# Optimization experiments

Measured on AMD Instinct MI355X. Metric: run time of the kernel, lower is better.

The kernel has to match this reference:

```python
import jax, jax.numpy as jnp
import numpy as np

DIM = 256
N_EMBED = 8192
DECAY = 0.99
EPS = 1e-05


def setup_inputs() -> dict:
    key = jax.random.key(0)
    k1, k2, k3, k4 = jax.random.split(key, 4)
    z = jax.random.normal(k1, (16, 32, 32, DIM), dtype=jnp.float32)
    embedding = jax.random.normal(k2, (DIM, N_EMBED), dtype=jnp.float32)
    cluster_size = jax.random.uniform(k3, (N_EMBED,), dtype=jnp.float32)
    embedding_avg = jax.random.normal(k4, (DIM, N_EMBED), dtype=jnp.float32)
    return {"z": z, "embedding": embedding, "cluster_size": cluster_size,
            "embedding_avg": embedding_avg}


def reference(z, embedding, cluster_size, embedding_avg):
    flatten = z.reshape(-1, DIM)  # [N, dim]
    dist = ((flatten ** 2).sum(1, keepdims=True)
            - 2.0 * flatten @ embedding
            + (embedding ** 2).sum(0, keepdims=True))
    embed_ind_flat = jnp.argmin(dist, axis=1)  # [N] int
    embed_ind = embed_ind_flat.reshape(z.shape[:-1])
    # Gather codes: embedding is [dim, n_embed]; quantize [..., dim]
    quantize = jnp.take(embedding.T, embed_ind_flat, axis=0).reshape(z.shape)

    # EMA codebook update (training path), via segment sums (no dense one-hot)
    onehot_sum = jax.ops.segment_sum(
        jnp.ones_like(embed_ind_flat, dtype=flatten.dtype),
        embed_ind_flat, num_segments=N_EMBED)  # [n_embed]
    embed_sum = jax.ops.segment_sum(flatten, embed_ind_flat,
                                    num_segments=N_EMBED).T  # [dim, n_embed]
    new_cluster_size = cluster_size * DECAY + (1.0 - DECAY) * onehot_sum
    new_embedding_avg = embedding_avg * DECAY + (1.0 - DECAY) * embed_sum
    n = new_cluster_size.sum()
    smoothed = (new_cluster_size + EPS) / (n + N_EMBED * EPS) * n
    new_embedding = new_embedding_avg / smoothed[None, :]

    diff = jnp.mean((jax.lax.stop_gradient(quantize) - z) ** 2)
    quantize_st = z + jax.lax.stop_gradient(quantize - z)
    return (quantize_st, diff, embed_ind, new_embedding,
            new_cluster_size, new_embedding_avg)
```

## Files before the change

kernel.cpp:

```cpp
#include <hip/hip_runtime.h>


#define DIMC  256
#define NEMB  8192
#define NROWS 16384

#define OUT_Q      0u
#define OUT_DIFF   4194304u
#define OUT_IDX    4194305u
#define OUT_NEWEMB 4210689u
#define OUT_NEWCS  6307841u
#define OUT_NEWAVG 6316033u

#define WS_EHI    0u
#define WS_ELO    1048576u
#define WS_COUNT  2097152u
#define WS_DIFF   2105344u
#define WS_N      2105345u
#define WS_ENORM  2105346u
#define WS_PACK   2113540u

typedef __attribute__((ext_vector_type(8))) short short8;
typedef __attribute__((ext_vector_type(4))) float f32x4;

__device__ inline void split_bf16(float x, unsigned short& h, unsigned short& l) {
  unsigned u = __float_as_uint(x);
  unsigned r = u + 0x7FFFu + ((u >> 16) & 1u);
  h = (unsigned short)(r >> 16);
  float hf = __uint_as_float((unsigned)h << 16);
  float lo = x - hf;
  unsigned u2 = __float_as_uint(lo);
  unsigned r2 = u2 + 0x7FFFu + ((u2 >> 16) & 1u);
  l = (unsigned short)(r2 >> 16);
}

__device__ inline float bf16_f(unsigned short u) {
  return __uint_as_float((unsigned)u << 16);
}

__global__ __launch_bounds__(256) void prep_kernel(
    const float* __restrict__ z, const float* __restrict__ emb,
    const float* __restrict__ cs, unsigned short* __restrict__ z_hi,
    unsigned short* __restrict__ z_lo, unsigned short* __restrict__ e_hi,
    unsigned short* __restrict__ e_lo, float* __restrict__ enorm,
    float* __restrict__ embsum, unsigned long long* __restrict__ pack,
    float* __restrict__ count_diff, float* __restrict__ n_out) {
  const int b = blockIdx.x;
  const int t = threadIdx.x;
  __shared__ float tile[64][68];
  __shared__ float red[4][64];

  if (b < 1024) {
#pragma unroll
    for (int it = 0; it < 4; ++it) {
      const int idx = (b * 256 + t) + it * 262144;
      const float4 v = reinterpret_cast<const float4*>(z)[idx];
      ushort4 h, l;
      split_bf16(v.x, h.x, l.x);
      split_bf16(v.y, h.y, l.y);
      split_bf16(v.z, h.z, l.z);
      split_bf16(v.w, h.w, l.w);
      reinterpret_cast<ushort4*>(z_hi)[idx] = h;
      reinterpret_cast<ushort4*>(z_lo)[idx] = l;
    }
  } else if (b < 1536) {
    const int bb = b - 1024;
    const int n0 = (bb & 127) * 64;
    const int k0 = (bb >> 7) * 64;
    const int c4 = (t & 15) * 4;
    const int rr = t >> 4;
#pragma unroll
    for (int i = 0; i < 4; ++i) {
      const int kl = rr + i * 16;
      const float4 v = *reinterpret_cast<const float4*>(
          &emb[(size_t)(k0 + kl) * NEMB + n0 + c4]);
      *reinterpret_cast<float4*>(&tile[kl][c4]) = v;
    }
    __syncthreads();
#pragma unroll
    for (int i = 0; i < 4; ++i) {
      const int nr = rr + i * 16;
      float4 v;
      v.x = tile[c4 + 0][nr];
      v.y = tile[c4 + 1][nr];
      v.z = tile[c4 + 2][nr];
      v.w = tile[c4 + 3][nr];
      const size_t off = (size_t)(n0 + nr) * DIMC + k0 + c4;
      ushort4 h, l;
      split_bf16(v.x, h.x, l.x);
      split_bf16(v.y, h.y, l.y);
      split_bf16(v.z, h.z, l.z);
      split_bf16(v.w, h.w, l.w);
      *reinterpret_cast<ushort4*>(&e_hi[off]) = h;
      *reinterpret_cast<ushort4*>(&e_lo[off]) = l;
    }
  } else if (b < 2048) {
    const int bb = b - 1536;
    const float4 zero = {0.f, 0.f, 0.f, 0.f};
#pragma unroll
    for (int it = 0; it < 4; ++it)
      reinterpret_cast<float4*>(embsum)[bb * 1024 + t + it * 256] = zero;
  } else if (b < 2176) {
    const int l = t & 63;
    const int dg = t >> 6;
    const int e = (b - 2048) * 64 + l;
    float s = 0.f;
#pragma unroll 8
    for (int d = dg * 64; d < dg * 64 + 64; ++d) {
      const float v = emb[(size_t)d * NEMB + e];
      s = fmaf(v, v, s);
    }
    red[dg][l] = s;
    __syncthreads();
    if (dg == 0) enorm[e] = red[0][l] + red[1][l] + red[2][l] + red[3][l];
  } else if (b < 2184) {
    const int bb = b - 2176;
    const uint4 ff = {~0u, ~0u, ~0u, ~0u};
#pragma unroll
    for (int it = 0; it < 4; ++it)
      reinterpret_cast<uint4*>(pack)[bb * 1024 + t + it * 256] = ff;
  } else if (b == 2184) {
    for (int i = t; i < 8193; i += 256) count_diff[i] = 0.f;
  } else {
    float s = 0.f;
#pragma unroll
    for (int i = 0; i < 32; ++i) s += cs[t + i * 256];
#pragma unroll
    for (int off = 32; off > 0; off >>= 1) s += __shfl_down(s, off, 64);
    if ((t & 63) == 0) red[0][t >> 6] = s;
    __syncthreads();
    if (t == 0)
      n_out[0] = 0.99f * (red[0][0] + red[0][1] + red[0][2] + red[0][3]) +
                 163.84f;
  }
}

__global__ __launch_bounds__(256, 2) void argmin_mfma_kernel(
    const unsigned short* __restrict__ z_hi, const unsigned short* __restrict__ z_lo,
    const unsigned short* __restrict__ e_hi, const unsigned short* __restrict__ e_lo,
    const float* __restrict__ enorm, unsigned long long* __restrict__ pack) {
  __shared__ short za[16384];
  __shared__ short eb[16384];
  __shared__ float elds[2048];
  const int tid = threadIdx.x;
  const int bid = blockIdx.x;
  const int xcd = bid & 7;
  const int w = bid >> 3;
  const int r0 = (xcd * 16 + (w & 15)) * 128;
  const int ebase = (w >> 4) * 2048;
  const int tx = tid & 15;
  const int q = (tid >> 4) & 3;
  const int wave = tid >> 6;
  const int wm = wave & 1;
  const int wn = wave >> 1;

  const unsigned zdel = (unsigned)(z_lo - z_hi);
  const unsigned edel = (unsigned)(e_lo - e_hi);

  const int lp = (tid & 7) ^ ((tid >> 3) & 7);
  const unsigned sz = (lp & 4) ? zdel : 0u;
  const unsigned se = (lp & 4) ? edel : 0u;
  const unsigned dch8 = (unsigned)(lp & 3) * 8u;
  unsigned zo[4], eo[4];
#pragma unroll
  for (int it = 0; it < 4; ++it) {
    const int row_it = (tid >> 3) + it * 32;
    zo[it] = sz + (unsigned)(r0 + row_it) * 256u + dch8;
    eo[it] = se + (unsigned)(ebase + row_it) * 256u + dch8;
  }

  auto STAGE = [&](int sidx) {
    const unsigned k0s = (unsigned)(sidx & 7) * 32u;
    const unsigned eas = (unsigned)(sidx >> 3) * 32768u + k0s;
    const unsigned lb = (unsigned)(sidx & 1) * 8192u + (unsigned)tid * 8u;
#pragma unroll
    for (int it = 0; it < 4; ++it) {
      __builtin_amdgcn_global_load_lds(
          (const __attribute__((address_space(1))) unsigned int*)(z_hi + zo[it] + k0s),
          (__attribute__((address_space(3))) unsigned int*)&za[lb + it * 2048],
          16, 0, 0);
      __builtin_amdgcn_global_load_lds(
          (const __attribute__((address_space(1))) unsigned int*)(e_hi + eo[it] + eas),
          (__attribute__((address_space(3))) unsigned int*)&eb[lb + it * 2048],
          16, 0, 0);
    }
  };

  float rmin[4][4];
  int ridx[4][4];
#pragma unroll
  for (int i = 0; i < 4; ++i)
#pragma unroll
    for (int r = 0; r < 4; ++r) { rmin[i][r] = 3.4028235e38f; ridx[i][r] = 0; }

  STAGE(0);
  {
    const float4 v0 = *reinterpret_cast<const float4*>(&enorm[ebase + tid * 8]);
    const float4 v1 =
        *reinterpret_cast<const float4*>(&enorm[ebase + tid * 8 + 4]);
    *reinterpret_cast<float4*>(&elds[tid * 8]) = v0;
    *reinterpret_cast<float4*>(&elds[tid * 8 + 4]) = v1;
  }
  __syncthreads();

  for (int nt = 0; nt < 16; ++nt) {
    f32x4 acc[4][4];
#pragma unroll
    for (int i = 0; i < 4; ++i)
#pragma unroll
      for (int j = 0; j < 4; ++j) acc[i][j] = (f32x4)0.0f;

    for (int k2 = 0; k2 < 8; ++k2) {
      const int s = nt * 8 + k2;
      if (s < 127) STAGE(s + 1);

      const short* zb = &za[(unsigned)(s & 1) * 8192u];
      const short* ebf = &eb[(unsigned)(s & 1) * 8192u];
      short8 ah[4], al[4], bh[4], bl[4];
#pragma unroll
      for (int i = 0; i < 4; ++i) {
        const int va = q ^ (tx & 7);
        const int rl = wm * 64 + i * 16 + tx;
        ah[i] = *reinterpret_cast<const short8*>(&zb[rl * 64 + va * 8]);
        al[i] = *reinterpret_cast<const short8*>(&zb[rl * 64 + (va ^ 4) * 8]);
        const int cl = wn * 64 + i * 16 + tx;
        bh[i] = *reinterpret_cast<const short8*>(&ebf[cl * 64 + va * 8]);
        bl[i] = *reinterpret_cast<const short8*>(&ebf[cl * 64 + (va ^ 4) * 8]);
      }
#pragma unroll
      for (int i = 0; i < 4; ++i)
#pragma unroll
        for (int j = 0; j < 4; ++j) {
          acc[i][j] = __builtin_amdgcn_mfma_f32_16x16x32_bf16(ah[i], bh[j],
                                                             acc[i][j], 0, 0, 0);
          acc[i][j] = __builtin_amdgcn_mfma_f32_16x16x32_bf16(ah[i], bl[j],
                                                             acc[i][j], 0, 0, 0);
          acc[i][j] = __builtin_amdgcn_mfma_f32_16x16x32_bf16(al[i], bh[j],
                                                             acc[i][j], 0, 0, 0);
        }

      asm volatile("s_waitcnt vmcnt(0) lgkmcnt(0)" ::: "memory");
      __builtin_amdgcn_sched_barrier(0);
      __builtin_amdgcn_s_barrier();
      asm volatile("" ::: "memory");
    }

#pragma unroll
    for (int j = 0; j < 4; ++j) {
      const int cidx = nt * 128 + wn * 64 + j * 16 + tx;
      const float en = elds[cidx];
      const int col = ebase + cidx;
#pragma unroll
      for (int i = 0; i < 4; ++i)
#pragma unroll
        for (int r = 0; r < 4; ++r) {
          const float sc = en - 2.0f * acc[i][j][r];
          if (sc < rmin[i][r]) { rmin[i][r] = sc; ridx[i][r] = col; }
        }
    }
  }

#pragma unroll
  for (int i = 0; i < 4; ++i)
#pragma unroll
    for (int r = 0; r < 4; ++r) {
      float v = rmin[i][r];
      int ix = ridx[i][r];
#pragma unroll
      for (int off = 1; off < 16; off <<= 1) {
        const float ov = __shfl_xor(v, off, 16);
        const int oi = __shfl_xor(ix, off, 16);
        if (ov < v || (ov == v && oi < ix)) { v = ov; ix = oi; }
      }
      if (tx == 0) {
        const unsigned int fb = __float_as_uint(v);
        const unsigned int sb = (fb & 0x80000000u) ? ~fb : (fb | 0x80000000u);
        const unsigned long long key =
            ((unsigned long long)sb << 13) | (unsigned long long)(unsigned)ix;
        atomicMin(&pack[r0 + wm * 64 + i * 16 + q * 4 + r], key);
      }
    }
}

__global__ __launch_bounds__(256) void gather_update_kernel(
    const float* __restrict__ z, const unsigned short* __restrict__ e_hi,
    const unsigned short* __restrict__ e_lo,
    const unsigned long long* __restrict__ pack, float* __restrict__ out_q,
    float* __restrict__ out_idx, float* __restrict__ embsum,
    float* __restrict__ count, float* __restrict__ diff_acc) {
  const int row = blockIdx.x * 4 + (threadIdx.x >> 6);
  const int lane = threadIdx.x & 63;
  const int e = (int)(pack[row] & 8191ULL);
  if (lane == 0) out_idx[row] = (float)e;
  const float4 zv =
      *reinterpret_cast<const float4*>(&z[(size_t)row * DIMC + lane * 4]);
  const ushort4 h =
      *reinterpret_cast<const ushort4*>(&e_hi[(size_t)e * DIMC + lane * 4]);
  const ushort4 l =
      *reinterpret_cast<const ushort4*>(&e_lo[(size_t)e * DIMC + lane * 4]);
  const float q0 = bf16_f(h.x) + bf16_f(l.x);
  const float q1 = bf16_f(h.y) + bf16_f(l.y);
  const float q2 = bf16_f(h.z) + bf16_f(l.z);
  const float q3 = bf16_f(h.w) + bf16_f(l.w);
  const float d0 = q0 - zv.x, d1 = q1 - zv.y, d2 = q2 - zv.z, d3 = q3 - zv.w;
  float4 st;
  st.x = zv.x + d0; st.y = zv.y + d1; st.z = zv.z + d2; st.w = zv.w + d3;
  *reinterpret_cast<float4*>(&out_q[(size_t)row * DIMC + lane * 4]) = st;

  atomicAdd(&embsum[(size_t)e * DIMC + lane * 4 + 0], zv.x);
  atomicAdd(&embsum[(size_t)e * DIMC + lane * 4 + 1], zv.y);
  atomicAdd(&embsum[(size_t)e * DIMC + lane * 4 + 2], zv.z);
  atomicAdd(&embsum[(size_t)e * DIMC + lane * 4 + 3], zv.w);

  float local = d0 * d0 + d1 * d1 + d2 * d2 + d3 * d3;
#pragma unroll
  for (int off = 32; off > 0; off >>= 1) local += __shfl_down(local, off, 64);

  __shared__ float dred[4];
  if (lane == 0) {
    dred[threadIdx.x >> 6] = local;
    atomicAdd(&count[e], 1.0f);
  }
  __syncthreads();
  if (threadIdx.x == 0)
    atomicAdd(diff_acc, dred[0] + dred[1] + dred[2] + dred[3]);
}

__global__ __launch_bounds__(256) void fin1_kernel(
    const float* __restrict__ eavg, const float* __restrict__ embsum,
    const float* __restrict__ cs, const float* __restrict__ count,
    const float* __restrict__ n_ptr, const float* __restrict__ diff_acc,
    float* __restrict__ out_emb, float* __restrict__ out_ncs,
    float* __restrict__ out_diff) {
  const int b = blockIdx.x;
  const int t = threadIdx.x;
  __shared__ float tile[64][68];
  __shared__ float rs[64];
  if (b < 512) {
    const int e0 = (b & 127) * 64;
    const int d0 = (b >> 7) * 64;
    const int c4 = (t & 15) * 4;
    const int rr = t >> 4;
    if (t < 64) {
      const float n = n_ptr[0];
      const float ncs = cs[e0 + t] * 0.99f + 0.01f * count[e0 + t];
      const float sm = (ncs + 1e-5f) / (n + 0.08192f) * n;
      rs[t] = 1.0f / sm;
    }
#pragma unroll
    for (int i = 0; i < 4; ++i) {
      const int er = rr + i * 16;
      const float4 v = *reinterpret_cast<const float4*>(
          &embsum[(size_t)(e0 + er) * DIMC + d0 + c4]);
      *reinterpret_cast<float4*>(&tile[er][c4]) = v;
    }
    __syncthreads();
#pragma unroll
    for (int i = 0; i < 4; ++i) {
      const int dr = rr + i * 16;
      const size_t g = (size_t)(d0 + dr) * NEMB + e0 + c4;
      const float4 av = *reinterpret_cast<const float4*>(&eavg[g]);
      float4 o;
      o.x = (av.x * 0.99f + 0.01f * tile[c4 + 0][dr]) * rs[c4 + 0];
      o.y = (av.y * 0.99f + 0.01f * tile[c4 + 1][dr]) * rs[c4 + 1];
      o.z = (av.z * 0.99f + 0.01f * tile[c4 + 2][dr]) * rs[c4 + 2];
      o.w = (av.w * 0.99f + 0.01f * tile[c4 + 3][dr]) * rs[c4 + 3];
      *reinterpret_cast<float4*>(&out_emb[g]) = o;
    }
  } else {
    const int g = (b - 512) * 256 + t;
    out_ncs[g] = cs[g] * 0.99f + 0.01f * count[g];
    if (g == 0) out_diff[0] = diff_acc[0] * (1.0f / 4194304.0f);
  }
}

__global__ __launch_bounds__(256) void fin2b_kernel(
    const float* __restrict__ cs, const float* __restrict__ count,
    const float* __restrict__ n_ptr, const float* __restrict__ out_emb,
    float* __restrict__ out_avg) {
  const int g = blockIdx.x * 256 + threadIdx.x;
  const int e = g & 8191;
  const float n = n_ptr[0];
  const float ncs = cs[e] * 0.99f + 0.01f * count[e];
  const float sm = (ncs + 1e-5f) / (n + 0.08192f) * n;
  out_avg[g] = out_emb[g] * sm;
}

extern "C" void kernel_launch(void* const* d_in, const int* in_sizes, int n_in,
                              void* d_out, int out_size, void* d_ws,
                              size_t ws_size, hipStream_t stream) {
  const float* z = (const float*)d_in[0];
  const float* emb = (const float*)d_in[1];
  const float* cs = (const float*)d_in[2];
  const float* eavg = (const float*)d_in[3];
  float* out = (float*)d_out;
  float* ws = (float*)d_ws;

  unsigned short* e_hi = (unsigned short*)(ws + WS_EHI);
  unsigned short* e_lo = (unsigned short*)(ws + WS_ELO);
  float* ws_count = ws + WS_COUNT;
  float* ws_diff = ws + WS_DIFF;
  float* ws_n = ws + WS_N;
  float* ws_enorm = ws + WS_ENORM;
  unsigned long long* ws_pack = (unsigned long long*)(ws + WS_PACK);

  unsigned short* z_hi = (unsigned short*)(out + OUT_Q);
  unsigned short* z_lo = (unsigned short*)(out + OUT_Q + 2097152);
  float* embsum = out + OUT_NEWAVG;

  prep_kernel<<<2186, 256, 0, stream>>>(z, emb, cs, z_hi, z_lo, e_hi, e_lo,
                                        ws_enorm, embsum, ws_pack, ws_count,
                                        ws_n);
  argmin_mfma_kernel<<<512, 256, 0, stream>>>(z_hi, z_lo, e_hi, e_lo, ws_enorm,
                                              ws_pack);
  gather_update_kernel<<<NROWS / 4, 256, 0, stream>>>(
      z, e_hi, e_lo, ws_pack, out + OUT_Q, out + OUT_IDX, embsum, ws_count,
      ws_diff);
  fin1_kernel<<<544, 256, 0, stream>>>(eavg, embsum, cs, ws_count, ws_n,
                                       ws_diff, out + OUT_NEWEMB,
                                       out + OUT_NEWCS, out + OUT_DIFF);
  fin2b_kernel<<<(DIMC * NEMB) / 256, 256, 0, stream>>>(
      cs, ws_count, ws_n, out + OUT_NEWEMB, out + OUT_NEWAVG);
}
```

Before: 384.9 us.

## Load codebook operands directly from global into registers, dropping LDS staging

The codebook (B) tiles are no longer staged through LDS. Each wave loads its bf16 hi/lo fragments directly from global memory into double-buffered registers one step ahead, while z still goes through LDS. The k2 loop is fully unrolled and the per-step wait drops the lgkmcnt and sched_barrier. This halves LDS footprint and traffic, which may allow more occupancy, but it duplicates global/L2 reads of the codebook across waves. Uncoalesced per-lane 16-byte loads and extra register pressure may also hurt. The final stage wraps around to prefetch redundant data instead of skipping.

Result: slower. 535.3 us (+39.1%).

```diff
diff --git a/kernel.cpp b/kernel.cpp
--- a/kernel.cpp
+++ b/kernel.cpp
@@ -140,7 +140,6 @@
     const unsigned short* __restrict__ e_hi, const unsigned short* __restrict__ e_lo,
     const float* __restrict__ enorm, unsigned long long* __restrict__ pack) {
   __shared__ short za[16384];
-  __shared__ short eb[16384];
   __shared__ float elds[2048];
   const int tid = threadIdx.x;
   const int bid = blockIdx.x;
@@ -153,25 +152,23 @@
   const int wave = tid >> 6;
   const int wm = wave & 1;
   const int wn = wave >> 1;
+  const int va = q ^ (tx & 7);
+  const unsigned qa8 = (unsigned)q * 8u;
 
   const unsigned zdel = (unsigned)(z_lo - z_hi);
-  const unsigned edel = (unsigned)(e_lo - e_hi);
 
   const int lp = (tid & 7) ^ ((tid >> 3) & 7);
   const unsigned sz = (lp & 4) ? zdel : 0u;
-  const unsigned se = (lp & 4) ? edel : 0u;
   const unsigned dch8 = (unsigned)(lp & 3) * 8u;
-  unsigned zo[4], eo[4];
+  unsigned zo[4];
 #pragma unroll
   for (int it = 0; it < 4; ++it) {
     const int row_it = (tid >> 3) + it * 32;
     zo[it] = sz + (unsigned)(r0 + row_it) * 256u + dch8;
-    eo[it] = se + (unsigned)(ebase + row_it) * 256u + dch8;
-  }
-
-  auto STAGE = [&](int sidx) {
+  }
+
+  auto STAGE_Z = [&](int sidx) {
     const unsigned k0s = (unsigned)(sidx & 7) * 32u;
-    const unsigned eas = (unsigned)(sidx >> 3) * 32768u + k0s;
     const unsigned lb = (unsigned)(sidx & 1) * 8192u + (unsigned)tid * 8u;
 #pragma unroll
     for (int it = 0; it < 4; ++it) {
@@ -179,10 +176,6 @@
           (const __attribute__((address_space(1))) unsigned int*)(z_hi + zo[it] + k0s),
           (__attribute__((address_space(3))) unsigned int*)&za[lb + it * 2048],
           16, 0, 0);
-      __builtin_amdgcn_global_load_lds(
-          (const __attribute__((address_space(1))) unsigned int*)(e_hi + eo[it] + eas),
-          (__attribute__((address_space(3))) unsigned int*)&eb[lb + it * 2048],
-          16, 0, 0);
     }
   };
 
@@ -193,7 +186,9 @@
 #pragma unroll
     for (int r = 0; r < 4; ++r) { rmin[i][r] = 3.4028235e38f; ridx[i][r] = 0; }
 
-  STAGE(0);
+  short8 pbh[2][4], pbl[2][4];
+
+  STAGE_Z(0);
   {
     const float4 v0 = *reinterpret_cast<const float4*>(&enorm[ebase + tid * 8]);
     const float4 v1 =
@@ -201,6 +196,15 @@
     *reinterpret_cast<float4*>(&elds[tid * 8]) = v0;
     *reinterpret_cast<float4*>(&elds[tid * 8 + 4]) = v1;
   }
+  {
+    const unsigned cb = (unsigned)(ebase + wn * 64);
+#pragma unroll
+    for (int j = 0; j < 4; ++j) {
+      const unsigned off = (cb + (unsigned)(j * 16 + tx)) * 256u + qa8;
+      pbh[0][j] = *reinterpret_cast<const short8*>(e_hi + off);
+      pbl[0][j] = *reinterpret_cast<const short8*>(e_lo + off);
+    }
+  }
   __syncthreads();
 
   for (int nt = 0; nt < 16; ++nt) {
@@ -210,37 +214,49 @@
 #pragma unroll
       for (int j = 0; j < 4; ++j) acc[i][j] = (f32x4)0.0f;
 
+#pragma unroll
     for (int k2 = 0; k2 < 8; ++k2) {
       const int s = nt * 8 + k2;
-      if (s < 127) STAGE(s + 1);
-
-      const short* zb = &za[(unsigned)(s & 1) * 8192u];
-      const short* ebf = &eb[(unsigned)(s & 1) * 8192u];
-      short8 ah[4], al[4], bh[4], bl[4];
+      const int cur = k2 & 1;
+      const int nxt = cur ^ 1;
+      const int s1 = (s + 1) & 127;
+
+      STAGE_Z(s1);
+
+      short8 ah[4], al[4];
+      const unsigned abase = (unsigned)cur * 8192u;
 #pragma unroll
       for (int i = 0; i < 4; ++i) {
-        const int va = q ^ (tx & 7);
-        const int rl = wm * 64 + i * 16 + tx;
-        ah[i] = *reinterpret_cast<const short8*>(&zb[rl * 64 + va * 8]);
-        al[i] = *reinterpret_cast<const short8*>(&zb[rl * 64 + (va ^ 4) * 8]);
-        const int cl = wn * 64 + i * 16 + tx;
-        bh[i] = *reinterpret_cast<const short8*>(&ebf[cl * 64 + va * 8]);
-        bl[i] = *reinterpret_cast<const short8*>(&ebf[cl * 64 + (va ^ 4) * 8]);
+        const unsigned rl = (unsigned)(wm * 64 + i * 16 + tx);
+        ah[i] = *reinterpret_cast<const short8*>(&za[abase + rl * 64u + (unsigned)va * 8u]);
+        al[i] = *reinterpret_cast<const short8*>(&za[abase + rl * 64u + (unsigned)(va ^ 4) * 8u]);
       }
+
+      {
+        const unsigned cb =
+            (unsigned)ebase + (unsigned)(s1 >> 3) * 128u + (unsigned)(wn * 64);
+        const unsigned k01 = (unsigned)(s1 & 7) * 32u;
+#pragma unroll
+        for (int j = 0; j < 4; ++j) {
+          const unsigned off = (cb + (unsigned)(j * 16 + tx)) * 256u + k01 + qa8;
+          pbh[nxt][j] = *reinterpret_cast<const short8*>(e_hi + off);
+          pbl[nxt][j] = *reinterpret_cast<const short8*>(e_lo + off);
+        }
+      }
+
 #pragma unroll
       for (int i = 0; i < 4; ++i)
 #pragma unroll
         for (int j = 0; j < 4; ++j) {
-          acc[i][j] = __builtin_amdgcn_mfma_f32_16x16x32_bf16(ah[i], bh[j],
+          acc[i][j] = __builtin_amdgcn_mfma_f32_16x16x32_bf16(ah[i], pbh[cur][j],
                                                              acc[i][j], 0, 0, 0);
-          acc[i][j] = __builtin_amdgcn_mfma_f32_16x16x32_bf16(ah[i], bl[j],
+          acc[i][j] = __builtin_amdgcn_mfma_f32_16x16x32_bf16(ah[i], pbl[cur][j],
                                                              acc[i][j], 0, 0, 0);
-          acc[i][j] = __builtin_amdgcn_mfma_f32_16x16x32_bf16(al[i], bh[j],
+          acc[i][j] = __builtin_amdgcn_mfma_f32_16x16x32_bf16(al[i], pbh[cur][j],
                                                              acc[i][j], 0, 0, 0);
         }
 
-      asm volatile("s_waitcnt vmcnt(0) lgkmcnt(0)" ::: "memory");
-      __builtin_amdgcn_sched_barrier(0);
+      asm volatile("s_waitcnt vmcnt(0)" ::: "memory");
       __builtin_amdgcn_s_barrier();
       asm volatile("" ::: "memory");
     }
```
